# Optimization experiments

Hardware: AMD Instinct MI355X
Metric: run time of the kernel (lower is better)

## Reference

```python
import jax, jax.numpy as jnp
import numpy as np

B, C, N, H = 4, 256, 1024, 8
D = C            # per-head q/k dim (out_channels defaults to in_channels)
DV = C           # per-head value/output dim (y_out_channels defaults to out_channels)


def setup_inputs() -> dict:
    key = jax.random.key(0)
    ks = jax.random.split(key, 10)
    s = 0.02
    return {
        "x": jax.random.normal(ks[0], (B, C, N), jnp.float32),
        "y": jax.random.normal(ks[1], (B, C, N), jnp.float32),
        "Wq": jax.random.normal(ks[2], (H * D, C), jnp.float32) * s,
        "bq": jnp.zeros((H * D,), jnp.float32),
        "Wk": jax.random.normal(ks[3], (H * D, C), jnp.float32) * s,
        "bk": jnp.zeros((H * D,), jnp.float32),
        "Wv": jax.random.normal(ks[4], (H * DV, C), jnp.float32) * s,
        "bv": jnp.zeros((H * DV,), jnp.float32),
        "Wp": jax.random.normal(ks[5], (DV, C), jnp.float32) * s,  # projection, bias=False
        "gamma": jax.random.uniform(ks[6], (H, 1, 1, 1), jnp.float32) + 0.001,
    }


def _pconv(t, W, b):
    # 1x1 conv1d: (O,C) x (B,C,N) -> (B,O,N)
    out = jnp.einsum('oc,bcn->bon', W, t)
    return out if b is None else out + b[None, :, None]


def reference(x, y, Wq, bq, Wk, bk, Wv, bv, Wp, gamma):
    b_, _, n_ = x.shape
    h = gamma.shape[0]
    # Q/K/V projections, split channels into h heads (head-major chunks of D)
    q = _pconv(x, Wq, bq).reshape(b_, h, -1, n_)   # [B,H,D,N]
    k = _pconv(x, Wk, bk).reshape(b_, h, -1, n_)   # [B,H,D,N]
    v = _pconv(y, Wv, bv).reshape(b_, h, -1, n_)   # [B,H,DV,N]
    # energy[i,j] = sum_d q[d,i]*k[d,j]; softmax over keys j (no sqrt(d) scaling)
    attn = jax.nn.softmax(jnp.einsum('bhdn,bhdm->bhnm', q, k), axis=-1)
    out = jnp.einsum('bhdm,bhnm->bhdn', v, attn)   # [B,H,DV,N]
    # residual branch: y projected to DV channels (1x1 conv, no bias)
    yp = jnp.einsum('oc,bcn->bon', Wp, y)          # [B,DV,N]
    g = gamma.reshape(1, h, 1, 1)
    out = (g * out + yp[:, None, :, :]) / (1.0 + g)
    # concat heads along channel dim (head-major), matching split_cat(out,1,0,2)
    return out.reshape(b_, -1, n_)                 # [B,H*DV,N]
```

## Files before the change

### kernel.cpp

```cpp
#include <hip/hip_runtime.h>

#define Bb 4
#define Cc 256
#define Nn 1024
#define Hh 8
#define Oo 2048

typedef __attribute__((ext_vector_type(8))) short bf16x8;
typedef __attribute__((ext_vector_type(4))) float f32x4;

__device__ __forceinline__ short f2bf(float f) {
  unsigned u = __builtin_bit_cast(unsigned, f);
  unsigned r = u + 0x7FFFu + ((u >> 16) & 1u);
  return (short)(r >> 16);
}
__device__ __forceinline__ f32x4 mfma16(bf16x8 a, bf16x8 b, f32x4 c) {
  return __builtin_amdgcn_mfma_f32_16x16x32_bf16(a, b, c, 0, 0, 0);
}
__device__ __forceinline__ void gl_lds16(const void* g, void* l) {
  __builtin_amdgcn_global_load_lds(
      (const __attribute__((address_space(1))) void*)g,
      (__attribute__((address_space(3))) void*)l, 16, 0, 0);
}

__device__ __forceinline__ void stage_row512(const char* gbase, char* lds,
                                             int wave, int lane) {
#pragma unroll
  for (int i = 0; i < 8; i++) {
    int off = (wave * 8 + i) * 1024;
    int L = off + lane * 16;
    int r = L >> 9;
    int c = ((L >> 4) & 31) ^ (r & 7);
    gl_lds16(gbase + r * 512 + c * 16, lds + off);
  }
}
__device__ __forceinline__ void stage_v(const char* Vg, char* lds, int k0,
                                        int wave, int lane) {
#pragma unroll
  for (int i = 0; i < 8; i++) {
    int off = (wave * 8 + i) * 1024;
    int L = off + lane * 16;
    int r = L >> 7;
    int c = ((L >> 4) & 7) ^ (r & 7);
    gl_lds16(Vg + (size_t)r * 2048 + k0 * 2 + c * 16, lds + off);
  }
}

__global__ __launch_bounds__(256) void k_transpose(
    const float* __restrict__ x, const float* __restrict__ y,
    short* __restrict__ xT, short* __restrict__ yT,
    const float* __restrict__ Wq, const float* __restrict__ Wk,
    const float* __restrict__ Wv, const float* __restrict__ Wp,
    short* __restrict__ dWq, short* __restrict__ dWk, short* __restrict__ dWv,
    short* __restrict__ dWp) {
  {
    const int NW = Oo * Cc;
    int lin = blockIdx.x + 16 * (blockIdx.y + 4 * blockIdx.z);
    for (int i = (lin * 256 + threadIdx.x) * 4; i < 3 * NW + Cc * Cc;
         i += 512 * 256 * 4) {
      const float* src;
      short* dst;
      int off;
      if (i < NW) {
        src = Wq; dst = dWq; off = i;
      } else if (i < 2 * NW) {
        src = Wk; dst = dWk; off = i - NW;
      } else if (i < 3 * NW) {
        src = Wv; dst = dWv; off = i - 2 * NW;
      } else {
        src = Wp; dst = dWp; off = i - 3 * NW;
      }
      float4 v = *(const float4*)(src + off);
      short4 o;
      o.x = f2bf(v.x);
      o.y = f2bf(v.y);
      o.z = f2bf(v.z);
      o.w = f2bf(v.w);
      *(short4*)(dst + off) = o;
    }
  }
  int bz = blockIdx.z;
  int b = bz >> 1;
  const float* src = (bz & 1) ? y : x;
  short* dst = (bz & 1) ? yT : xT;
  src += (size_t)b * Cc * Nn;
  dst += (size_t)b * Nn * Cc;
  __shared__ short tile[64][72];
  int n0 = blockIdx.x * 64, c0 = blockIdx.y * 64;
  int t = threadIdx.x;
#pragma unroll
  for (int i = 0; i < 16; i++) {
    int idx = t + i * 256;
    int cc = idx >> 6, nn = idx & 63;
    tile[cc][nn] = f2bf(src[(size_t)(c0 + cc) * Nn + n0 + nn]);
  }
  __syncthreads();
#pragma unroll
  for (int i = 0; i < 16; i++) {
    int idx = t + i * 256;
    int nn = idx >> 6, cc = idx & 63;
    dst[(size_t)(n0 + nn) * Cc + c0 + cc] = tile[cc][nn];
  }
}

__global__ __launch_bounds__(256) void k_proj(
    const short* __restrict__ xT, const short* __restrict__ yT,
    const short* __restrict__ Wq, const float* __restrict__ bq,
    const short* __restrict__ Wk, const float* __restrict__ bk,
    const short* __restrict__ Wv, const float* __restrict__ bv,
    const short* __restrict__ Wp, short* __restrict__ Qt,
    short* __restrict__ Kt, short* __restrict__ Vv, float* __restrict__ yp) {
  int b = blockIdx.z, n0 = blockIdx.x * 64, by = blockIdx.y;
  int wave = threadIdx.x >> 6, lane = threadIdx.x & 63;
  int quad = lane >> 4, l16 = lane & 15;
  int sw = l16 & 7;
  __shared__ short S1[64 * 256];
  __shared__ short S2[64 * 256];

  if (by < 32) {
    int o0 = by * 64;
    stage_row512((const char*)(Wq + (size_t)o0 * Cc), (char*)S1, wave, lane);
    stage_row512((const char*)(Wk + (size_t)o0 * Cc), (char*)S2, wave, lane);
    const short* aptr = xT + (size_t)b * Nn * Cc +
                        (size_t)(n0 + wave * 16 + l16) * Cc + quad * 8;
    bf16x8 areg[8];
#pragma unroll
    for (int ks = 0; ks < 8; ks++) areg[ks] = *(const bf16x8*)(aptr + ks * 32);

    f32x4 accQ[4], accK[4];
#pragma unroll
    for (int j = 0; j < 4; j++) {
      accQ[j] = f32x4{0.f, 0.f, 0.f, 0.f};
      accK[j] = f32x4{0.f, 0.f, 0.f, 0.f};
    }
    __syncthreads();
#pragma unroll
    for (int ks = 0; ks < 8; ks++) {
#pragma unroll
      for (int cj = 0; cj < 4; cj++) {
        int off = (cj * 16 + l16) * 512 + (((ks * 4 + quad) ^ sw) << 4);
        bf16x8 wqf = *(const bf16x8*)((const char*)S1 + off);
        bf16x8 wkf = *(const bf16x8*)((const char*)S2 + off);
        accQ[cj] = mfma16(areg[ks], wqf, accQ[cj]);
        accK[cj] = mfma16(areg[ks], wkf, accK[cj]);
      }
    }
#pragma unroll
    for (int cj = 0; cj < 4; cj++) {
      int o = o0 + cj * 16 + l16;
      int h = o >> 8, d = o & 255;
      float vbq = bq[o];
      float vbk = bk[o];
#pragma unroll
      for (int r = 0; r < 4; r++) {
        int n = n0 + wave * 16 + quad * 4 + r;
        size_t idx = (((size_t)(b * Hh + h) * Nn) + n) * 256 + d;
        Qt[idx] = f2bf(accQ[cj][r] + vbq);
        Kt[idx] = f2bf(accK[cj][r] + vbk);
      }
    }
  } else {
    bool isP = by >= 64;
    const short* W = isP ? Wp : Wv;
    int o0 = (isP ? (by - 64) : (by - 32)) * 64;
    stage_row512((const char*)(yT + (size_t)b * Nn * Cc + (size_t)n0 * Cc),
                 (char*)S1, wave, lane);
    const short* aptr = W + (size_t)(o0 + wave * 16 + l16) * Cc + quad * 8;
    bf16x8 areg[8];
#pragma unroll
    for (int ks = 0; ks < 8; ks++) areg[ks] = *(const bf16x8*)(aptr + ks * 32);

    f32x4 acc[4];
#pragma unroll
    for (int j = 0; j < 4; j++) acc[j] = f32x4{0.f, 0.f, 0.f, 0.f};
    __syncthreads();
#pragma unroll
    for (int ks = 0; ks < 8; ks++) {
#pragma unroll
      for (int cj = 0; cj < 4; cj++) {
        bf16x8 bb = *(const bf16x8*)((const char*)S1 + (cj * 16 + l16) * 512 +
                                     (((ks * 4 + quad) ^ sw) << 4));
        acc[cj] = mfma16(areg[ks], bb, acc[cj]);
      }
    }
#pragma unroll
    for (int cj = 0; cj < 4; cj++) {
      int n = n0 + cj * 16 + l16;
#pragma unroll
      for (int r = 0; r < 4; r++) {
        int o = o0 + wave * 16 + quad * 4 + r;
        if (isP) {
          yp[((size_t)b * Cc + o) * Nn + n] = acc[cj][r];
        } else {
          Vv[((size_t)b * Oo + o) * Nn + n] = f2bf(acc[cj][r] + bv[o]);
        }
      }
    }
  }
}

__global__ __launch_bounds__(256) void k_attn(
    const short* __restrict__ Qt, const short* __restrict__ Kt,
    const short* __restrict__ Vv, const float* __restrict__ yp,
    const float* __restrict__ gamma, float* __restrict__ out) {
  int id = blockIdx.x;
  int bh = (id & 7) * 4 + (id >> 7);
  int q0 = ((id >> 3) & 15) * 64;
  int b = bh >> 3, h = bh & 7;
  int wave = threadIdx.x >> 6, lane = threadIdx.x & 63;
  int quad = lane >> 4, l16 = lane & 15;
  int sw = l16 & 7;
  const short* Qb = Qt + (size_t)bh * Nn * 256;
  const char* Kg = (const char*)(Kt + (size_t)bh * Nn * 256);
  const char* Vg = (const char*)(Vv + (size_t)bh * 256 * Nn);

  __shared__ short Klds[64 * 256];
  __shared__ short Vlds[256 * 64];
  __shared__ short plds[4][16][64];
  __shared__ float llds[64];

  bf16x8 qreg[8];
  {
    const short* qp = Qb + (size_t)(q0 + wave * 16 + l16) * 256 + quad * 8;
#pragma unroll
    for (int ks = 0; ks < 8; ks++) qreg[ks] = *(const bf16x8*)(qp + ks * 32);
  }
  f32x4 oacc[16];
#pragma unroll
  for (int j = 0; j < 16; j++) oacc[j] = f32x4{0.f, 0.f, 0.f, 0.f};
  float l_i[4] = {0.f, 0.f, 0.f, 0.f};

  stage_row512(Kg, (char*)Klds, wave, lane);
  stage_v(Vg, (char*)Vlds, 0, wave, lane);

  for (int kt = 0; kt < 16; kt++) {
    int k0 = kt * 64;
    __syncthreads();
    f32x4 sc[4];
#pragma unroll
    for (int j = 0; j < 4; j++) sc[j] = f32x4{0.f, 0.f, 0.f, 0.f};
#pragma unroll
    for (int ks = 0; ks < 8; ks++) {
#pragma unroll
      for (int cj = 0; cj < 4; cj++) {
        bf16x8 kb = *(const bf16x8*)((const char*)Klds +
                                     (cj * 16 + l16) * 512 +
                                     (((ks * 4 + quad) ^ sw) << 4));
        sc[cj] = mfma16(qreg[ks], kb, sc[cj]);
      }
    }
#pragma unroll
    for (int cj = 0; cj < 4; cj++) {
#pragma unroll
      for (int r = 0; r < 4; r++) {
        float p = __expf(sc[cj][r]);
        l_i[r] += p;
        int row = quad * 4 + r;
        int s = (row & 7) ^ ((row >> 3) << 1);
        plds[wave][row][(((cj * 2 + (l16 >> 3)) ^ s) << 3) | sw] = f2bf(p);
      }
    }
    __syncthreads();
    if (kt < 15)
      stage_row512(Kg + (size_t)(k0 + 64) * 512, (char*)Klds, wave, lane);
    int sr = (l16 & 7) ^ ((l16 >> 3) << 1);
    bf16x8 ap0[4], ap1[4];
#pragma unroll
    for (int qb = 0; qb < 4; qb++) {
      ap0[qb] = *(const bf16x8*)&plds[qb][l16][(quad ^ sr) << 3];
      ap1[qb] = *(const bf16x8*)&plds[qb][l16][((quad + 4) ^ sr) << 3];
    }
#pragma unroll
    for (int dj = 0; dj < 4; dj++) {
      const char* vrow = (const char*)Vlds + (wave * 64 + dj * 16 + l16) * 128;
      bf16x8 v0 = *(const bf16x8*)(vrow + ((quad ^ sw) << 4));
      bf16x8 v1 = *(const bf16x8*)(vrow + (((quad + 4) ^ sw) << 4));
#pragma unroll
      for (int qb = 0; qb < 4; qb++) {
        oacc[qb * 4 + dj] = mfma16(ap0[qb], v0, oacc[qb * 4 + dj]);
        oacc[qb * 4 + dj] = mfma16(ap1[qb], v1, oacc[qb * 4 + dj]);
      }
    }
    __syncthreads();
    if (kt < 15) stage_v(Vg, (char*)Vlds, k0 + 64, wave, lane);
  }
#pragma unroll
  for (int r = 0; r < 4; r++) {
    float v = l_i[r];
    v += __shfl_xor(v, 1);
    v += __shfl_xor(v, 2);
    v += __shfl_xor(v, 4);
    v += __shfl_xor(v, 8);
    l_i[r] = v;
  }
  if (l16 == 0) {
    f32x4 lv;
#pragma unroll
    for (int r = 0; r < 4; r++) lv[r] = l_i[r];
    *(f32x4*)&llds[wave * 16 + quad * 4] = lv;
  }
  __syncthreads();
  float gf = gamma[h];
  float sg = gf / (1.f + gf), sy = 1.f / (1.f + gf);
#pragma unroll
  for (int qb = 0; qb < 4; qb++) {
    f32x4 lv = *(const f32x4*)&llds[qb * 16 + quad * 4];
    int qq = q0 + qb * 16 + quad * 4;
#pragma unroll
    for (int dj = 0; dj < 4; dj++) {
      int dv = wave * 64 + dj * 16 + l16;
      const float* ypp = yp + ((size_t)b * 256 + dv) * Nn + qq;
      float* op = out + ((size_t)b * Oo + h * 256 + dv) * Nn + qq;
      float4 yv = *(const float4*)ypp;
      f32x4 oa = oacc[qb * 4 + dj];
      float4 ov;
      ov.x = sg * (oa[0] / lv[0]) + sy * yv.x;
      ov.y = sg * (oa[1] / lv[1]) + sy * yv.y;
      ov.z = sg * (oa[2] / lv[2]) + sy * yv.z;
      ov.w = sg * (oa[3] / lv[3]) + sy * yv.w;
      *(float4*)op = ov;
    }
  }
}

extern "C" void kernel_launch(void* const* d_in, const int* in_sizes, int n_in,
                              void* d_out, int out_size, void* d_ws,
                              size_t ws_size, hipStream_t stream) {
  const float* x = (const float*)d_in[0];
  const float* y = (const float*)d_in[1];
  const float* Wq = (const float*)d_in[2];
  const float* bq = (const float*)d_in[3];
  const float* Wk = (const float*)d_in[4];
  const float* bk = (const float*)d_in[5];
  const float* Wv = (const float*)d_in[6];
  const float* bv = (const float*)d_in[7];
  const float* Wp = (const float*)d_in[8];
  const float* gamma = (const float*)d_in[9];
  float* out = (float*)d_out;

  char* w = (char*)d_ws;
  short* Qt = (short*)(w + 0);
  short* Kt = (short*)(w + 16777216);
  short* Vv = (short*)(w + 33554432);
  short* xT = (short*)(w + 50331648);
  short* yT = (short*)(w + 52428800);
  float* yp = (float*)(w + 54525952);
  short* Wqb = (short*)(w + 58720256);
  short* Wkb = (short*)(w + 59768832);
  short* Wvb = (short*)(w + 60817408);
  short* Wpb = (short*)(w + 61865984);

  k_transpose<<<dim3(Nn / 64, Cc / 64, 2 * Bb), dim3(256), 0, stream>>>(
      x, y, xT, yT, Wq, Wk, Wv, Wp, Wqb, Wkb, Wvb, Wpb);
  k_proj<<<dim3(Nn / 64, 68, Bb), dim3(256), 0, stream>>>(
      xT, yT, Wqb, bq, Wkb, bk, Wvb, bv, Wpb, Qt, Kt, Vv, yp);
  k_attn<<<dim3(512), dim3(256), 0, stream>>>(Qt, Kt, Vv, yp, gamma, out);
}
```

Before: 199.6 us.

## Persistent proj blocks reuse staged weights; split attn scores across 2x2 wave grid

k_proj moves from a 3D grid of 4352 blocks to 512 blocks. Each block keeps one staged LDS tile (the Wq/Wk rows, or the y tile) and loops over several n-tiles or output tiles, prefetching the next register operand. This cuts redundant LDS staging of weights and launch overhead, at the cost of less parallelism per block. In k_attn, each wave now computes a 32-query by 32-key quadrant of the score tile instead of 16 queries by 64 keys, so every K fragment read from LDS feeds two MFMAs. The row sums are then kept as two partial halves that are added at normalization.

Measured after the change: 207.2 us. 3.8% more time.

```diff
diff --git a/kernel.cpp b/kernel.cpp
--- a/kernel.cpp
+++ b/kernel.cpp
@@ -110,91 +110,134 @@
     const short* __restrict__ Wv, const float* __restrict__ bv,
     const short* __restrict__ Wp, short* __restrict__ Qt,
     short* __restrict__ Kt, short* __restrict__ Vv, float* __restrict__ yp) {
-  int b = blockIdx.z, n0 = blockIdx.x * 64, by = blockIdx.y;
   int wave = threadIdx.x >> 6, lane = threadIdx.x & 63;
   int quad = lane >> 4, l16 = lane & 15;
   int sw = l16 & 7;
   __shared__ short S1[64 * 256];
   __shared__ short S2[64 * 256];
-
-  if (by < 32) {
-    int o0 = by * 64;
+  int id = blockIdx.x;
+
+  if (id < 256) {
+    int ot = id >> 3, b = (id >> 1) & 3, nhalf = id & 1;
+    int o0 = ot * 64;
     stage_row512((const char*)(Wq + (size_t)o0 * Cc), (char*)S1, wave, lane);
     stage_row512((const char*)(Wk + (size_t)o0 * Cc), (char*)S2, wave, lane);
-    const short* aptr = xT + (size_t)b * Nn * Cc +
-                        (size_t)(n0 + wave * 16 + l16) * Cc + quad * 8;
-    bf16x8 areg[8];
-#pragma unroll
-    for (int ks = 0; ks < 8; ks++) areg[ks] = *(const bf16x8*)(aptr + ks * 32);
-
-    f32x4 accQ[4], accK[4];
-#pragma unroll
-    for (int j = 0; j < 4; j++) {
-      accQ[j] = f32x4{0.f, 0.f, 0.f, 0.f};
-      accK[j] = f32x4{0.f, 0.f, 0.f, 0.f};
+    float vbq[4], vbk[4];
+#pragma unroll
+    for (int cj = 0; cj < 4; cj++) {
+      vbq[cj] = bq[o0 + cj * 16 + l16];
+      vbk[cj] = bk[o0 + cj * 16 + l16];
+    }
+    const short* xbase = xT + (size_t)b * Nn * Cc;
+    bf16x8 areg[8], aregN[8];
+    {
+      const short* ap =
+          xbase + (size_t)(nhalf * 512 + wave * 16 + l16) * Cc + quad * 8;
+#pragma unroll
+      for (int ks = 0; ks < 8; ks++) areg[ks] = *(const bf16x8*)(ap + ks * 32);
     }
     __syncthreads();
-#pragma unroll
-    for (int ks = 0; ks < 8; ks++) {
+#pragma unroll 1
+    for (int i = 0; i < 8; i++) {
+      int ncur = nhalf * 512 + i * 64;
+      if (i < 7) {
+        const short* ap =
+            xbase + (size_t)(ncur + 64 + wave * 16 + l16) * Cc + quad * 8;
+#pragma unroll
+        for (int ks = 0; ks < 8; ks++)
+          aregN[ks] = *(const bf16x8*)(ap + ks * 32);
+      }
+      f32x4 accQ[4], accK[4];
+#pragma unroll
+      for (int j = 0; j < 4; j++) {
+        accQ[j] = f32x4{0.f, 0.f, 0.f, 0.f};
+        accK[j] = f32x4{0.f, 0.f, 0.f, 0.f};
+      }
+#pragma unroll
+      for (int ks = 0; ks < 8; ks++) {
+#pragma unroll
+        for (int cj = 0; cj < 4; cj++) {
+          int off = (cj * 16 + l16) * 512 + (((ks * 4 + quad) ^ sw) << 4);
+          bf16x8 wqf = *(const bf16x8*)((const char*)S1 + off);
+          bf16x8 wkf = *(const bf16x8*)((const char*)S2 + off);
+          accQ[cj] = mfma16(areg[ks], wqf, accQ[cj]);
+          accK[cj] = mfma16(areg[ks], wkf, accK[cj]);
+        }
+      }
 #pragma unroll
       for (int cj = 0; cj < 4; cj++) {
-        int off = (cj * 16 + l16) * 512 + (((ks * 4 + quad) ^ sw) << 4);
-        bf16x8 wqf = *(const bf16x8*)((const char*)S1 + off);
-        bf16x8 wkf = *(const bf16x8*)((const char*)S2 + off);
-        accQ[cj] = mfma16(areg[ks], wqf, accQ[cj]);
-        accK[cj] = mfma16(areg[ks], wkf, accK[cj]);
-      }
-    }
-#pragma unroll
-    for (int cj = 0; cj < 4; cj++) {
-      int o = o0 + cj * 16 + l16;
-      int h = o >> 8, d = o & 255;
-      float vbq = bq[o];
-      float vbk = bk[o];
-#pragma unroll
-      for (int r = 0; r < 4; r++) {
-        int n = n0 + wave * 16 + quad * 4 + r;
-        size_t idx = (((size_t)(b * Hh + h) * Nn) + n) * 256 + d;
-        Qt[idx] = f2bf(accQ[cj][r] + vbq);
-        Kt[idx] = f2bf(accK[cj][r] + vbk);
-      }
+        int o = o0 + cj * 16 + l16;
+        int h = o >> 8, d = o & 255;
+#pragma unroll
+        for (int r = 0; r < 4; r++) {
+          int n = ncur + wave * 16 + quad * 4 + r;
+          size_t idx = (((size_t)(b * Hh + h) * Nn) + n) * 256 + d;
+          Qt[idx] = f2bf(accQ[cj][r] + vbq[cj]);
+          Kt[idx] = f2bf(accK[cj][r] + vbk[cj]);
+        }
+      }
+#pragma unroll
+      for (int ks = 0; ks < 8; ks++) areg[ks] = aregN[ks];
     }
   } else {
-    bool isP = by >= 64;
-    const short* W = isP ? Wp : Wv;
-    int o0 = (isP ? (by - 64) : (by - 32)) * 64;
+    int id2 = id - 256;
+    int nt = id2 >> 4, b = (id2 >> 2) & 3, oq = id2 & 3;
+    int n0 = nt * 64;
     stage_row512((const char*)(yT + (size_t)b * Nn * Cc + (size_t)n0 * Cc),
                  (char*)S1, wave, lane);
-    const short* aptr = W + (size_t)(o0 + wave * 16 + l16) * Cc + quad * 8;
-    bf16x8 areg[8];
-#pragma unroll
-    for (int ks = 0; ks < 8; ks++) areg[ks] = *(const bf16x8*)(aptr + ks * 32);
-
-    f32x4 acc[4];
-#pragma unroll
-    for (int j = 0; j < 4; j++) acc[j] = f32x4{0.f, 0.f, 0.f, 0.f};
+    bf16x8 areg[8], aregN[8];
+    {
+      int ot = oq * 9;
+      const short* wb = (ot < 32) ? (Wv + (size_t)ot * 64 * Cc)
+                                  : (Wp + (size_t)(ot - 32) * 64 * Cc);
+      const short* ap = wb + (size_t)(wave * 16 + l16) * Cc + quad * 8;
+#pragma unroll
+      for (int ks = 0; ks < 8; ks++) areg[ks] = *(const bf16x8*)(ap + ks * 32);
+    }
     __syncthreads();
-#pragma unroll
-    for (int ks = 0; ks < 8; ks++) {
+#pragma unroll 1
+    for (int j = 0; j < 9; j++) {
+      int ot = oq * 9 + j;
+      bool isP = ot >= 32;
+      int o0 = (isP ? ot - 32 : ot) * 64;
+      if (j < 8) {
+        int otn = ot + 1;
+        const short* wb = (otn < 32) ? (Wv + (size_t)otn * 64 * Cc)
+                                     : (Wp + (size_t)(otn - 32) * 64 * Cc);
+        const short* ap = wb + (size_t)(wave * 16 + l16) * Cc + quad * 8;
+#pragma unroll
+        for (int ks = 0; ks < 8; ks++)
+          aregN[ks] = *(const bf16x8*)(ap + ks * 32);
+      }
+      float4 bvv = *(const float4*)&bv[o0 + wave * 16 + quad * 4];
+      f32x4 acc[4];
+#pragma unroll
+      for (int jj = 0; jj < 4; jj++) acc[jj] = f32x4{0.f, 0.f, 0.f, 0.f};
+#pragma unroll
+      for (int ks = 0; ks < 8; ks++) {
+#pragma unroll
+        for (int cj = 0; cj < 4; cj++) {
+          bf16x8 bb = *(const bf16x8*)((const char*)S1 + (cj * 16 + l16) * 512 +
+                                       (((ks * 4 + quad) ^ sw) << 4));
+          acc[cj] = mfma16(areg[ks], bb, acc[cj]);
+        }
+      }
 #pragma unroll
       for (int cj = 0; cj < 4; cj++) {
-        bf16x8 bb = *(const bf16x8*)((const char*)S1 + (cj * 16 + l16) * 512 +
-                                     (((ks * 4 + quad) ^ sw) << 4));
-        acc[cj] = mfma16(areg[ks], bb, acc[cj]);
-      }
-    }
-#pragma unroll
-    for (int cj = 0; cj < 4; cj++) {
-      int n = n0 + cj * 16 + l16;
-#pragma unroll
-      for (int r = 0; r < 4; r++) {
-        int o = o0 + wave * 16 + quad * 4 + r;
-        if (isP) {
-          yp[((size_t)b * Cc + o) * Nn + n] = acc[cj][r];
-        } else {
-          Vv[((size_t)b * Oo + o) * Nn + n] = f2bf(acc[cj][r] + bv[o]);
+        int n = n0 + cj * 16 + l16;
+#pragma unroll
+        for (int r = 0; r < 4; r++) {
+          int o = o0 + wave * 16 + quad * 4 + r;
+          if (isP) {
+            yp[((size_t)b * Cc + o) * Nn + n] = acc[cj][r];
+          } else {
+            float bvr = (r == 0) ? bvv.x : (r == 1) ? bvv.y : (r == 2) ? bvv.z : bvv.w;
+            Vv[((size_t)b * Oo + o) * Nn + n] = f2bf(acc[cj][r] + bvr);
+          }
         }
       }
+#pragma unroll
+      for (int ks = 0; ks < 8; ks++) areg[ks] = aregN[ks];
     }
   }
 }
@@ -210,25 +253,29 @@
   int wave = threadIdx.x >> 6, lane = threadIdx.x & 63;
   int quad = lane >> 4, l16 = lane & 15;
   int sw = l16 & 7;
+  int qh = wave & 1, kh = wave >> 1;
   const short* Qb = Qt + (size_t)bh * Nn * 256;
   const char* Kg = (const char*)(Kt + (size_t)bh * Nn * 256);
   const char* Vg = (const char*)(Vv + (size_t)bh * 256 * Nn);
 
   __shared__ short Klds[64 * 256];
   __shared__ short Vlds[256 * 64];
-  __shared__ short plds[4][16][64];
-  __shared__ float llds[64];
-
-  bf16x8 qreg[8];
-  {
-    const short* qp = Qb + (size_t)(q0 + wave * 16 + l16) * 256 + quad * 8;
-#pragma unroll
-    for (int ks = 0; ks < 8; ks++) qreg[ks] = *(const bf16x8*)(qp + ks * 32);
+  __shared__ short plds[64][64];
+  __shared__ float llds[2][64];
+
+  bf16x8 qreg[2][8];
+#pragma unroll
+  for (int qb2 = 0; qb2 < 2; qb2++) {
+    const short* qp =
+        Qb + (size_t)(q0 + qh * 32 + qb2 * 16 + l16) * 256 + quad * 8;
+#pragma unroll
+    for (int ks = 0; ks < 8; ks++)
+      qreg[qb2][ks] = *(const bf16x8*)(qp + ks * 32);
   }
   f32x4 oacc[16];
 #pragma unroll
   for (int j = 0; j < 16; j++) oacc[j] = f32x4{0.f, 0.f, 0.f, 0.f};
-  float l_i[4] = {0.f, 0.f, 0.f, 0.f};
+  float l_i[2][4] = {{0.f, 0.f, 0.f, 0.f}, {0.f, 0.f, 0.f, 0.f}};
 
   stage_row512(Kg, (char*)Klds, wave, lane);
   stage_v(Vg, (char*)Vlds, 0, wave, lane);
@@ -236,39 +283,45 @@
   for (int kt = 0; kt < 16; kt++) {
     int k0 = kt * 64;
     __syncthreads();
-    f32x4 sc[4];
-#pragma unroll
-    for (int j = 0; j < 4; j++) sc[j] = f32x4{0.f, 0.f, 0.f, 0.f};
+    f32x4 sc[2][2];
+#pragma unroll
+    for (int a = 0; a < 2; a++)
+#pragma unroll
+      for (int c = 0; c < 2; c++) sc[a][c] = f32x4{0.f, 0.f, 0.f, 0.f};
 #pragma unroll
     for (int ks = 0; ks < 8; ks++) {
-#pragma unroll
-      for (int cj = 0; cj < 4; cj++) {
-        bf16x8 kb = *(const bf16x8*)((const char*)Klds +
-                                     (cj * 16 + l16) * 512 +
-                                     (((ks * 4 + quad) ^ sw) << 4));
-        sc[cj] = mfma16(qreg[ks], kb, sc[cj]);
-      }
-    }
-#pragma unroll
-    for (int cj = 0; cj < 4; cj++) {
-#pragma unroll
-      for (int r = 0; r < 4; r++) {
-        float p = __expf(sc[cj][r]);
-        l_i[r] += p;
-        int row = quad * 4 + r;
-        int s = (row & 7) ^ ((row >> 3) << 1);
-        plds[wave][row][(((cj * 2 + (l16 >> 3)) ^ s) << 3) | sw] = f2bf(p);
+      int chnk = ((ks * 4 + quad) ^ sw) << 4;
+      bf16x8 kb0 =
+          *(const bf16x8*)((const char*)Klds + (kh * 32 + l16) * 512 + chnk);
+      bf16x8 kb1 = *(const bf16x8*)((const char*)Klds +
+                                    (kh * 32 + 16 + l16) * 512 + chnk);
+      sc[0][0] = mfma16(qreg[0][ks], kb0, sc[0][0]);
+      sc[0][1] = mfma16(qreg[0][ks], kb1, sc[0][1]);
+      sc[1][0] = mfma16(qreg[1][ks], kb0, sc[1][0]);
+      sc[1][1] = mfma16(qreg[1][ks], kb1, sc[1][1]);
+    }
+#pragma unroll
+    for (int qb2 = 0; qb2 < 2; qb2++) {
+#pragma unroll
+      for (int cj2 = 0; cj2 < 2; cj2++) {
+#pragma unroll
+        for (int r = 0; r < 4; r++) {
+          float p = __expf(sc[qb2][cj2][r]);
+          l_i[qb2][r] += p;
+          int row = qh * 32 + qb2 * 16 + quad * 4 + r;
+          int key = kh * 32 + cj2 * 16 + l16;
+          plds[row][((((key >> 3) ^ (row & 7))) << 3) | (key & 7)] = f2bf(p);
+        }
       }
     }
     __syncthreads();
     if (kt < 15)
       stage_row512(Kg + (size_t)(k0 + 64) * 512, (char*)Klds, wave, lane);
-    int sr = (l16 & 7) ^ ((l16 >> 3) << 1);
     bf16x8 ap0[4], ap1[4];
 #pragma unroll
     for (int qb = 0; qb < 4; qb++) {
-      ap0[qb] = *(const bf16x8*)&plds[qb][l16][(quad ^ sr) << 3];
-      ap1[qb] = *(const bf16x8*)&plds[qb][l16][((quad + 4) ^ sr) << 3];
+      ap0[qb] = *(const bf16x8*)&plds[qb * 16 + l16][(quad ^ sw) << 3];
+      ap1[qb] = *(const bf16x8*)&plds[qb * 16 + l16][((quad + 4) ^ sw) << 3];
     }
 #pragma unroll
     for (int dj = 0; dj < 4; dj++) {
@@ -285,26 +338,33 @@
     if (kt < 15) stage_v(Vg, (char*)Vlds, k0 + 64, wave, lane);
   }
 #pragma unroll
-  for (int r = 0; r < 4; r++) {
-    float v = l_i[r];
-    v += __shfl_xor(v, 1);
-    v += __shfl_xor(v, 2);
-    v += __shfl_xor(v, 4);
-    v += __shfl_xor(v, 8);
-    l_i[r] = v;
+  for (int qb2 = 0; qb2 < 2; qb2++) {
+#pragma unroll
+    for (int r = 0; r < 4; r++) {
+      float v = l_i[qb2][r];
+      v += __shfl_xor(v, 1);
+      v += __shfl_xor(v, 2);
+      v += __shfl_xor(v, 4);
+      v += __shfl_xor(v, 8);
+      l_i[qb2][r] = v;
+    }
   }
   if (l16 == 0) {
-    f32x4 lv;
-#pragma unroll
-    for (int r = 0; r < 4; r++) lv[r] = l_i[r];
-    *(f32x4*)&llds[wave * 16 + quad * 4] = lv;
+#pragma unroll
+    for (int qb2 = 0; qb2 < 2; qb2++) {
+      f32x4 lv;
+#pragma unroll
+      for (int r = 0; r < 4; r++) lv[r] = l_i[qb2][r];
+      *(f32x4*)&llds[kh][qh * 32 + qb2 * 16 + quad * 4] = lv;
+    }
   }
   __syncthreads();
   float gf = gamma[h];
   float sg = gf / (1.f + gf), sy = 1.f / (1.f + gf);
 #pragma unroll
   for (int qb = 0; qb < 4; qb++) {
-    f32x4 lv = *(const f32x4*)&llds[qb * 16 + quad * 4];
+    f32x4 lv0 = *(const f32x4*)&llds[0][qb * 16 + quad * 4];
+    f32x4 lv1 = *(const f32x4*)&llds[1][qb * 16 + quad * 4];
     int qq = q0 + qb * 16 + quad * 4;
 #pragma unroll
     for (int dj = 0; dj < 4; dj++) {
@@ -314,10 +374,10 @@
       float4 yv = *(const float4*)ypp;
       f32x4 oa = oacc[qb * 4 + dj];
       float4 ov;
-      ov.x = sg * (oa[0] / lv[0]) + sy * yv.x;
-      ov.y = sg * (oa[1] / lv[1]) + sy * yv.y;
-      ov.z = sg * (oa[2] / lv[2]) + sy * yv.z;
-      ov.w = sg * (oa[3] / lv[3]) + sy * yv.w;
+      ov.x = sg * (oa[0] / (lv0[0] + lv1[0])) + sy * yv.x;
+      ov.y = sg * (oa[1] / (lv0[1] + lv1[1])) + sy * yv.y;
+      ov.z = sg * (oa[2] / (lv0[2] + lv1[2])) + sy * yv.z;
+      ov.w = sg * (oa[3] / (lv0[3] + lv1[3])) + sy * yv.w;
       *(float4*)op = ov;
     }
   }
@@ -352,7 +412,7 @@
 
   k_transpose<<<dim3(Nn / 64, Cc / 64, 2 * Bb), dim3(256), 0, stream>>>(
       x, y, xT, yT, Wq, Wk, Wv, Wp, Wqb, Wkb, Wvb, Wpb);
-  k_proj<<<dim3(Nn / 64, 68, Bb), dim3(256), 0, stream>>>(
+  k_proj<<<dim3(512), dim3(256), 0, stream>>>(
       xT, yT, Wqb, bq, Wkb, bk, Wvb, bv, Wpb, Qt, Kt, Vv, yp);
   k_attn<<<dim3(512), dim3(256), 0, stream>>>(Qt, Kt, Vv, yp, gamma, out);
 }
```
